# Optimization experiments

Measured on AMD Instinct MI355X. Metric: run time of the kernel, lower is better.

The kernel has to match this reference:

```python
import jax, jax.numpy as jnp
import numpy as np

N_EMBD = 1024
N_HEAD = 16
HEAD_DIM = N_EMBD // N_HEAD
EPS = 1e-5


def setup_inputs() -> dict:
    key = jax.random.key(0)
    ks = jax.random.split(key, 6)
    B, S, D = 2, 2048, N_EMBD
    s = 0.02
    return {
        "x": jax.random.normal(ks[0], (B, S, D), jnp.float32),
        "ln1_g": jnp.ones((D,), jnp.float32),
        "ln1_b": jnp.zeros((D,), jnp.float32),
        "w_attn": jax.random.normal(ks[1], (D, 3 * D), jnp.float32) * s,
        "b_attn": jnp.zeros((3 * D,), jnp.float32),
        "w_attn_proj": jax.random.normal(ks[2], (D, D), jnp.float32) * s,
        "b_attn_proj": jnp.zeros((D,), jnp.float32),
        "ln2_g": jnp.ones((D,), jnp.float32),
        "ln2_b": jnp.zeros((D,), jnp.float32),
        "w_fc": jax.random.normal(ks[3], (D, 4 * D), jnp.float32) * s,
        "b_fc": jnp.zeros((4 * D,), jnp.float32),
        "w_fc_proj": jax.random.normal(ks[4], (4 * D, D), jnp.float32) * s,
        "b_fc_proj": jnp.zeros((D,), jnp.float32),
    }


def _layernorm(x, g, b):
    mu = jnp.mean(x, axis=-1, keepdims=True)
    var = jnp.mean(jnp.square(x - mu), axis=-1, keepdims=True)
    return (x - mu) * jax.lax.rsqrt(var + EPS) * g + b


def _block(x, ln1_g, ln1_b, w_attn, b_attn, w_attn_proj, b_attn_proj,
           ln2_g, ln2_b, w_fc, b_fc, w_fc_proj, b_fc_proj):
    B, S, D = x.shape
    h = _layernorm(x, ln1_g, ln1_b)
    qkv = h @ w_attn + b_attn                       # [B,S,3D]
    q, k, v = jnp.split(qkv, 3, axis=-1)
    # [B,H,S,hd]
    q = q.reshape(B, S, N_HEAD, HEAD_DIM).transpose(0, 2, 1, 3)
    k = k.reshape(B, S, N_HEAD, HEAD_DIM).transpose(0, 2, 1, 3)
    v = v.reshape(B, S, N_HEAD, HEAD_DIM).transpose(0, 2, 1, 3)
    scores = jnp.einsum("bhqd,bhkd->bhqk", q, k) / jnp.sqrt(
        jnp.asarray(HEAD_DIM, x.dtype))
    causal = jnp.tril(jnp.ones((S, S), bool))
    scores = jnp.where(causal, scores, -jnp.inf)
    attn = jax.nn.softmax(scores, axis=-1)
    out = jnp.einsum("bhqk,bhkd->bhqd", attn, v)    # [B,H,S,hd]
    out = out.transpose(0, 2, 1, 3).reshape(B, S, D)
    x = x + (out @ w_attn_proj + b_attn_proj)
    h2 = _layernorm(x, ln2_g, ln2_b)
    m = jax.nn.gelu(h2 @ w_fc + b_fc, approximate=False)
    x = x + (m @ w_fc_proj + b_fc_proj)
    return x


def reference(x, ln1_g, ln1_b, w_attn, b_attn, w_attn_proj, b_attn_proj,
              ln2_g, ln2_b, w_fc, b_fc, w_fc_proj, b_fc_proj):
    return _block(x, ln1_g, ln1_b, w_attn, b_attn, w_attn_proj, b_attn_proj,
                  ln2_g, ln2_b, w_fc, b_fc, w_fc_proj, b_fc_proj)
```

## Files before the change

kernel.cpp:

```cpp
#include <hip/hip_runtime.h>
#include <hip/hip_bf16.h>
#include <math.h>

typedef __bf16 bf16_t;
typedef bf16_t bf16x8 __attribute__((ext_vector_type(8)));
typedef float f32x4 __attribute__((ext_vector_type(4)));
typedef unsigned short u16;
typedef u16 ushort8 __attribute__((ext_vector_type(8)));

static __device__ __forceinline__ u16 f2bf(float f) {
    unsigned u = __builtin_bit_cast(unsigned, f);
    u += 0x7FFFu + ((u >> 16) & 1u);
    return (u16)(u >> 16);
}

__global__ __launch_bounds__(256) void ln_kernel(
    const float* __restrict__ x, const float* __restrict__ g,
    const float* __restrict__ be, u16* __restrict__ out)
{
    const int row = blockIdx.x;
    const int tid = threadIdx.x;
    const float4 v = ((const float4*)(x + (long)row * 1024))[tid];
    float s = v.x + v.y + v.z + v.w;
#pragma unroll
    for (int d = 32; d >= 1; d >>= 1) s += __shfl_xor(s, d);
    __shared__ float r1[4], r2[4];
    if ((tid & 63) == 0) r1[tid >> 6] = s;
    __syncthreads();
    const float mean = (r1[0] + r1[1] + r1[2] + r1[3]) * (1.0f / 1024.0f);
    const float dx = v.x - mean, dy = v.y - mean, dz = v.z - mean, dw = v.w - mean;
    float sq = dx * dx + dy * dy + dz * dz + dw * dw;
#pragma unroll
    for (int d = 32; d >= 1; d >>= 1) sq += __shfl_xor(sq, d);
    if ((tid & 63) == 0) r2[tid >> 6] = sq;
    __syncthreads();
    const float var = (r2[0] + r2[1] + r2[2] + r2[3]) * (1.0f / 1024.0f);
    const float rstd = rsqrtf(var + 1e-5f);
    const float4 gg = ((const float4*)g)[tid];
    const float4 bb = ((const float4*)be)[tid];
    ushort4 o;
    o.x = f2bf(dx * rstd * gg.x + bb.x);
    o.y = f2bf(dy * rstd * gg.y + bb.y);
    o.z = f2bf(dz * rstd * gg.z + bb.z);
    o.w = f2bf(dw * rstd * gg.w + bb.w);
    *(ushort4*)&out[(long)row * 1024 + tid * 4] = o;
}

__global__ __launch_bounds__(256) void tcvt_kernel(
    const float* __restrict__ in, u16* __restrict__ outT, int R, int C)
{
    __shared__ float tile[32][33];
    const int tx = threadIdx.x, ty = threadIdx.y;
    const int c0 = blockIdx.x * 32, r0 = blockIdx.y * 32;
#pragma unroll
    for (int i = 0; i < 4; ++i)
        tile[ty + i * 8][tx] = in[(long)(r0 + ty + i * 8) * C + c0 + tx];
    __syncthreads();
#pragma unroll
    for (int i = 0; i < 4; ++i)
        outT[(long)(c0 + ty + i * 8) * R + r0 + tx] = f2bf(tile[tx][ty + i * 8]);
}

template <int BM, int EPI, int DP>
static __device__ __forceinline__ void gemm_body(
    const u16* __restrict__ A, const u16* __restrict__ Bt,
    const float* __restrict__ bias, const float* __restrict__ resid,
    void* __restrict__ C, int M, int N, int K)
{
    constexpr int WN = (BM == 128) ? 2 : 4;
    constexpr int MR = 4;
    constexpr int NR = 128 / WN / 16;
    constexpr int AI = BM / 64;
    constexpr int LPW = AI + 2;
    __shared__ __align__(16) u16 As[DP][BM * 32];
    __shared__ __align__(16) u16 Bs[DP][128 * 32];
    const int tid = threadIdx.x;
    const int lane = tid & 63;
    const int w = tid >> 6;
    const int wm = w / WN, wn = w % WN;
    const int nwg = gridDim.x * gridDim.y;
    const int flat = blockIdx.x + gridDim.x * blockIdx.y;
    const int work = (flat & 7) * (nwg >> 3) + (flat >> 3);
    const int bm = work % gridDim.x, bn = work / gridDim.x;
    f32x4 acc[MR][NR] = {};

    const u16* Ablk = A + (long)bm * BM * K;
    const u16* Bblk = Bt + (long)bn * 128 * K;
    const int nt = K >> 5;

    auto stage = [&](int buf, int kb) {
#pragma unroll
        for (int i = 0; i < AI; ++i) {
            const int o = (w * AI + i) * 512 + lane * 8;
            const int row = o >> 5, kk = o & 31;
            __builtin_amdgcn_global_load_lds(
                (const __attribute__((address_space(1))) void*)(Ablk + (long)row * K + kb + kk),
                (__attribute__((address_space(3))) void*)(&As[buf][(w * AI + i) * 512]),
                16, 0, 0);
        }
#pragma unroll
        for (int i = 0; i < 2; ++i) {
            const int o = (w * 2 + i) * 512 + lane * 8;
            const int row = o >> 5, kk = o & 31;
            __builtin_amdgcn_global_load_lds(
                (const __attribute__((address_space(1))) void*)(Bblk + (long)row * K + kb + kk),
                (__attribute__((address_space(3))) void*)(&Bs[buf][(w * 2 + i) * 512]),
                16, 0, 0);
        }
    };

#pragma unroll
    for (int s = 0; s < DP - 1; ++s) stage(s, s << 5);

    for (int t = 0; t < nt; ++t) {
        const int cur = t % DP;
        if (t + DP - 2 < nt) {
            asm volatile("s_waitcnt vmcnt(%0)" :: "i"((DP - 2) * LPW) : "memory");
        } else if (t + 1 < nt) {
            asm volatile("s_waitcnt vmcnt(%0)" :: "i"(LPW) : "memory");
        } else {
            asm volatile("s_waitcnt vmcnt(0)" ::: "memory");
        }
        __builtin_amdgcn_s_barrier();
        asm volatile("" ::: "memory");

        if (t + DP - 1 < nt) stage((t + DP - 1) % DP, (t + DP - 1) << 5);

        bf16x8 af[MR], bfr[NR];
#pragma unroll
        for (int m = 0; m < MR; ++m)
            af[m] = *(const bf16x8*)&As[cur][(wm * MR * 16 + m * 16 + (lane & 15)) * 32 + (lane >> 4) * 8];
#pragma unroll
        for (int n = 0; n < NR; ++n)
            bfr[n] = *(const bf16x8*)&Bs[cur][(wn * NR * 16 + n * 16 + (lane & 15)) * 32 + (lane >> 4) * 8];
#pragma unroll
        for (int m = 0; m < MR; ++m)
#pragma unroll
            for (int n = 0; n < NR; ++n)
                acc[m][n] = __builtin_amdgcn_mfma_f32_16x16x32_bf16(af[m], bfr[n], acc[m][n], 0, 0, 0);
        asm volatile("" ::: "memory");
    }

    const int rowBase = bm * BM + wm * MR * 16;
    const int colBase = bn * 128 + wn * NR * 16;
#pragma unroll
    for (int n = 0; n < NR; ++n) {
        const int col = colBase + n * 16 + (lane & 15);
        const float bv = bias[col];
#pragma unroll
        for (int m = 0; m < MR; ++m) {
#pragma unroll
            for (int r = 0; r < 4; ++r) {
                const int row = rowBase + m * 16 + (lane >> 4) * 4 + r;
                float v = acc[m][n][r] + bv;
                if constexpr (EPI == 1) {
                    const float u = v + 0.044715f * v * v * v;
                    v = v / (1.0f + __expf(-1.5957691216057308f * u));
                }
                if constexpr (EPI == 3) {
                    if (col < 1024) v *= 0.125f;
                }
                if constexpr (EPI == 2) {
                    ((float*)C)[(long)row * N + col] = v + resid[(long)row * N + col];
                } else {
                    ((u16*)C)[(long)row * N + col] = f2bf(v);
                }
            }
        }
    }
}

__global__ __launch_bounds__(256) void gemm_qkv(
    const u16* A, const u16* Bt, const float* bias, const float* resid,
    void* C, int M, int N, int K) { gemm_body<128, 3, 3>(A, Bt, bias, resid, C, M, N, K); }
__global__ __launch_bounds__(256) void gemm_fc(
    const u16* A, const u16* Bt, const float* bias, const float* resid,
    void* C, int M, int N, int K) { gemm_body<128, 1, 3>(A, Bt, bias, resid, C, M, N, K); }
__global__ __launch_bounds__(256) void gemm_ap(
    const u16* A, const u16* Bt, const float* bias, const float* resid,
    void* C, int M, int N, int K) { gemm_body<64, 2, 4>(A, Bt, bias, resid, C, M, N, K); }
__global__ __launch_bounds__(256) void gemm_fp(
    const u16* A, const u16* Bt, const float* bias, const float* resid,
    void* C, int M, int N, int K) { gemm_body<64, 2, 4>(A, Bt, bias, resid, C, M, N, K); }

__global__ __launch_bounds__(256) void attn_kernel(
    const u16* __restrict__ qkv, u16* __restrict__ outb)
{
    const int S = 2048;
    const int flat = blockIdx.x + 16 * blockIdx.y;
    const int work = (flat & 7) * 64 + (flat >> 3);
    const int ipair = work & 15;
    const int bh = work >> 4;
    const int b = bh >> 4, h = bh & 15;
    const int tid = threadIdx.x, lane = tid & 63, w = tid >> 6;
    __shared__ __align__(16) u16 Ks[2][64 * 72];
    __shared__ __align__(16) u16 Vs[2][64 * 72];
    __shared__ __align__(16) u16 Ps[4][16 * 72];

    const long base = (long)b * S * 3072;
    const int rstage = tid >> 3;
    const int cg = (tid & 7) * 8;
    const int sw = cg;
    const u16* kbase = qkv + base + 1024 + h * 64 + cg;
    const u16* vbase = qkv + base + 2048 + h * 64 + cg;

    for (int half = 0; half < 2; ++half) {
        const int qt = half ? 31 - ipair : ipair;
        const int q0 = qt * 64;

        bf16x8 qf[2];
        {
            const int qrow = q0 + w * 16 + (lane & 15);
#pragma unroll
            for (int c = 0; c < 2; ++c)
                qf[c] = *(const bf16x8*)&qkv[base + (long)qrow * 3072 + h * 64 + c * 32 + (lane >> 4) * 8];
        }

        f32x4 Of[4] = {};
        float m = -1e30f, l = 0.0f;

        ushort8 kr[2], vr[2];
#pragma unroll
        for (int it = 0; it < 2; ++it) {
            const long ro = (long)(it * 32 + rstage) * 3072;
            kr[it] = *(const ushort8*)&kbase[ro];
            vr[it] = *(const ushort8*)&vbase[ro];
        }
        __syncthreads();
#pragma unroll
        for (int it = 0; it < 2; ++it) {
            const int r = it * 32 + rstage;
            *(ushort8*)&Ks[0][r * 72 + cg] = kr[it];
#pragma unroll
            for (int j = 0; j < 8; ++j)
                Vs[0][(cg + j) * 72 + (r ^ sw)] = vr[it][j];
        }

        for (int kt = 0; kt <= qt; ++kt) {
            const int cur = kt & 1;
            if (kt < qt) {
#pragma unroll
                for (int it = 0; it < 2; ++it) {
                    const long ro = (long)((kt + 1) * 64 + it * 32 + rstage) * 3072;
                    kr[it] = *(const ushort8*)&kbase[ro];
                    vr[it] = *(const ushort8*)&vbase[ro];
                }
            }
            __syncthreads();

            f32x4 Sf[4] = {};
#pragma unroll
            for (int f = 0; f < 4; ++f) {
#pragma unroll
                for (int c = 0; c < 2; ++c) {
                    const bf16x8 kf = *(const bf16x8*)&Ks[cur][(f * 16 + (lane & 15)) * 72 + c * 32 + (lane >> 4) * 8];
                    Sf[f] = __builtin_amdgcn_mfma_f32_16x16x32_bf16(kf, qf[c], Sf[f], 0, 0, 0);
                }
            }
            if (kt == qt) {
                const int ql = w * 16 + (lane & 15);
#pragma unroll
                for (int f = 0; f < 4; ++f) {
#pragma unroll
                    for (int r = 0; r < 4; ++r) {
                        const int kvl = f * 16 + ((lane >> 4) << 2) + r;
                        if (kvl > ql) Sf[f][r] = -1e30f;
                    }
                }
            }
            float pmax = Sf[0][0];
#pragma unroll
            for (int f = 0; f < 4; ++f)
#pragma unroll
                for (int r = 0; r < 4; ++r) pmax = fmaxf(pmax, Sf[f][r]);
            if (!__all(pmax <= m + 8.0f)) {
                float pm = pmax;
                pm = fmaxf(pm, __shfl_xor(pm, 16));
                pm = fmaxf(pm, __shfl_xor(pm, 32));
                const float mnew = fmaxf(m, pm);
                const float sc = __expf(m - mnew);
                m = mnew;
                l *= sc;
                float sco[4];
#pragma unroll
                for (int r = 0; r < 4; ++r)
                    sco[r] = __shfl(sc, ((lane >> 4) << 2) + r);
#pragma unroll
                for (int f = 0; f < 4; ++f)
#pragma unroll
                    for (int r = 0; r < 4; ++r) Of[f][r] *= sco[r];
            }
            float osum = 0.0f;
#pragma unroll
            for (int f = 0; f < 4; ++f)
#pragma unroll
                for (int r = 0; r < 4; ++r) {
                    const float e = __expf(Sf[f][r] - m);
                    Sf[f][r] = e;
                    osum += e;
                }
            l += osum;
#pragma unroll
            for (int f = 0; f < 4; ++f) {
                const unsigned lo = (unsigned)f2bf(Sf[f][0]) | ((unsigned)f2bf(Sf[f][1]) << 16);
                const unsigned hi = (unsigned)f2bf(Sf[f][2]) | ((unsigned)f2bf(Sf[f][3]) << 16);
                uint2 pk; pk.x = lo; pk.y = hi;
                *(uint2*)&Ps[w][(lane & 15) * 72 + f * 16 + ((lane >> 4) << 2)] = pk;
            }
#pragma unroll
            for (int f = 0; f < 4; ++f) {
                const int hd = f * 16 + (lane & 15);
#pragma unroll
                for (int c = 0; c < 2; ++c) {
                    const int k0 = c * 32 + (lane >> 4) * 8;
                    const bf16x8 pa = *(const bf16x8*)&Ps[w][(lane & 15) * 72 + k0];
                    const bf16x8 vb = *(const bf16x8*)&Vs[cur][hd * 72 + (k0 ^ (hd & 56))];
                    Of[f] = __builtin_amdgcn_mfma_f32_16x16x32_bf16(pa, vb, Of[f], 0, 0, 0);
                }
            }
            if (kt < qt) {
#pragma unroll
                for (int it = 0; it < 2; ++it) {
                    const int r = it * 32 + rstage;
                    *(ushort8*)&Ks[cur ^ 1][r * 72 + cg] = kr[it];
#pragma unroll
                    for (int j = 0; j < 8; ++j)
                        Vs[cur ^ 1][(cg + j) * 72 + (r ^ sw)] = vr[it][j];
                }
            }
        }

        float lt = l;
        lt += __shfl_xor(lt, 16);
        lt += __shfl_xor(lt, 32);
        const float linv = 1.0f / lt;
        float inv[4];
#pragma unroll
        for (int r = 0; r < 4; ++r)
            inv[r] = __shfl(linv, ((lane >> 4) << 2) + r);
#pragma unroll
        for (int f = 0; f < 4; ++f) {
            const int col = h * 64 + f * 16 + (lane & 15);
#pragma unroll
            for (int r = 0; r < 4; ++r) {
                const int qrow = q0 + w * 16 + (lane >> 4) * 4 + r;
                outb[((long)b * S + qrow) * 1024 + col] = f2bf(Of[f][r] * inv[r]);
            }
        }
    }
}

extern "C" void kernel_launch(void* const* d_in, const int* in_sizes, int n_in,
                              void* d_out, int out_size, void* d_ws, size_t ws_size,
                              hipStream_t stream) {
    const float* x      = (const float*)d_in[0];
    const float* ln1_g  = (const float*)d_in[1];
    const float* ln1_b  = (const float*)d_in[2];
    const float* w_attn = (const float*)d_in[3];
    const float* b_attn = (const float*)d_in[4];
    const float* w_ap   = (const float*)d_in[5];
    const float* b_ap   = (const float*)d_in[6];
    const float* ln2_g  = (const float*)d_in[7];
    const float* ln2_b  = (const float*)d_in[8];
    const float* w_fc   = (const float*)d_in[9];
    const float* b_fc   = (const float*)d_in[10];
    const float* w_fp   = (const float*)d_in[11];
    const float* b_fp   = (const float*)d_in[12];
    float* out = (float*)d_out;

    const int R = 4096;
    char* p = (char*)d_ws;
    u16*   wTa  = (u16*)(p);
    u16*   wTap = (u16*)(p + 6291456);
    u16*   wTfc = (u16*)(p + 8388608);
    u16*   wTfp = (u16*)(p + 16777216);
    u16*   hao  = (u16*)(p + 25165824);
    u16*   qkv  = (u16*)(p + 33554432);
    u16*   mb   = hao;
    u16*   h2   = wTa;
    float* x1   = out;

    const dim3 tb(32, 8);
    tcvt_kernel<<<dim3(3072 / 32, 1024 / 32), tb, 0, stream>>>(w_attn, wTa, 1024, 3072);
    tcvt_kernel<<<dim3(1024 / 32, 1024 / 32), tb, 0, stream>>>(w_ap, wTap, 1024, 1024);
    tcvt_kernel<<<dim3(4096 / 32, 1024 / 32), tb, 0, stream>>>(w_fc, wTfc, 1024, 4096);
    tcvt_kernel<<<dim3(1024 / 32, 4096 / 32), tb, 0, stream>>>(w_fp, wTfp, 4096, 1024);

    ln_kernel<<<R, 256, 0, stream>>>(x, ln1_g, ln1_b, hao);
    gemm_qkv<<<dim3(32, 24), 256, 0, stream>>>(hao, wTa, b_attn, nullptr, qkv, R, 3072, 1024);
    attn_kernel<<<dim3(16, 32), 256, 0, stream>>>(qkv, hao);
    gemm_ap<<<dim3(64, 8), 256, 0, stream>>>(hao, wTap, b_ap, x, x1, R, 1024, 1024);
    ln_kernel<<<R, 256, 0, stream>>>(x1, ln2_g, ln2_b, h2);
    gemm_fc<<<dim3(32, 32), 256, 0, stream>>>(h2, wTfc, b_fc, nullptr, mb, R, 4096, 1024);
    gemm_fp<<<dim3(64, 8), 256, 0, stream>>>(mb, wTfp, b_fp, x1, out, R, 1024, 4096);
}
```

Before: 271.0 us.

## Stream B operand directly to registers in 64-row GEMMs, drop tile swizzle

The 64-row output-projection GEMMs get a new body. Each wave now loads its own 32 columns of B straight from global memory into registers with inline assembly, double-buffered, while only A is staged through LDS with two buffers instead of four. The 128-row GEMM is specialised to fixed constants, and the grouped workgroup remapping used for L2 locality is removed from both paths in favour of plain blockIdx order. This aims to cut LDS traffic and barrier cost for the skinny GEMMs, but it risks exposed global-load latency and worse L2 reuse without the swizzle.

New measurement: 271.3 us. About the same (+0.1%).

```diff
diff --git a/kernel.cpp b/kernel.cpp
--- a/kernel.cpp
+++ b/kernel.cpp
@@ -61,47 +61,36 @@
         outT[(long)(c0 + ty + i * 8) * R + r0 + tx] = f2bf(tile[tx][ty + i * 8]);
 }
 
-template <int BM, int EPI, int DP>
-static __device__ __forceinline__ void gemm_body(
+template <int EPI, int DP>
+static __device__ __forceinline__ void gemm128_body(
     const u16* __restrict__ A, const u16* __restrict__ Bt,
     const float* __restrict__ bias, const float* __restrict__ resid,
     void* __restrict__ C, int M, int N, int K)
 {
-    constexpr int WN = (BM == 128) ? 2 : 4;
-    constexpr int MR = 4;
-    constexpr int NR = 128 / WN / 16;
-    constexpr int AI = BM / 64;
-    constexpr int LPW = AI + 2;
-    __shared__ __align__(16) u16 As[DP][BM * 32];
+    constexpr int MR = 4, NR = 4;
+    constexpr int LPW = 4;
+    __shared__ __align__(16) u16 As[DP][128 * 32];
     __shared__ __align__(16) u16 Bs[DP][128 * 32];
     const int tid = threadIdx.x;
     const int lane = tid & 63;
     const int w = tid >> 6;
-    const int wm = w / WN, wn = w % WN;
-    const int nwg = gridDim.x * gridDim.y;
-    const int flat = blockIdx.x + gridDim.x * blockIdx.y;
-    const int work = (flat & 7) * (nwg >> 3) + (flat >> 3);
-    const int bm = work % gridDim.x, bn = work / gridDim.x;
+    const int wm = w >> 1, wn = w & 1;
+    const int bm = blockIdx.x, bn = blockIdx.y;
     f32x4 acc[MR][NR] = {};
 
-    const u16* Ablk = A + (long)bm * BM * K;
+    const u16* Ablk = A + (long)bm * 128 * K;
     const u16* Bblk = Bt + (long)bn * 128 * K;
     const int nt = K >> 5;
 
     auto stage = [&](int buf, int kb) {
 #pragma unroll
-        for (int i = 0; i < AI; ++i) {
-            const int o = (w * AI + i) * 512 + lane * 8;
+        for (int i = 0; i < 2; ++i) {
+            const int o = (w * 2 + i) * 512 + lane * 8;
             const int row = o >> 5, kk = o & 31;
             __builtin_amdgcn_global_load_lds(
                 (const __attribute__((address_space(1))) void*)(Ablk + (long)row * K + kb + kk),
-                (__attribute__((address_space(3))) void*)(&As[buf][(w * AI + i) * 512]),
+                (__attribute__((address_space(3))) void*)(&As[buf][(w * 2 + i) * 512]),
                 16, 0, 0);
-        }
-#pragma unroll
-        for (int i = 0; i < 2; ++i) {
-            const int o = (w * 2 + i) * 512 + lane * 8;
-            const int row = o >> 5, kk = o & 31;
             __builtin_amdgcn_global_load_lds(
                 (const __attribute__((address_space(1))) void*)(Bblk + (long)row * K + kb + kk),
                 (__attribute__((address_space(3))) void*)(&Bs[buf][(w * 2 + i) * 512]),
@@ -129,10 +118,10 @@
         bf16x8 af[MR], bfr[NR];
 #pragma unroll
         for (int m = 0; m < MR; ++m)
-            af[m] = *(const bf16x8*)&As[cur][(wm * MR * 16 + m * 16 + (lane & 15)) * 32 + (lane >> 4) * 8];
+            af[m] = *(const bf16x8*)&As[cur][(wm * 64 + m * 16 + (lane & 15)) * 32 + (lane >> 4) * 8];
 #pragma unroll
         for (int n = 0; n < NR; ++n)
-            bfr[n] = *(const bf16x8*)&Bs[cur][(wn * NR * 16 + n * 16 + (lane & 15)) * 32 + (lane >> 4) * 8];
+            bfr[n] = *(const bf16x8*)&Bs[cur][(wn * 64 + n * 16 + (lane & 15)) * 32 + (lane >> 4) * 8];
 #pragma unroll
         for (int m = 0; m < MR; ++m)
 #pragma unroll
@@ -141,8 +130,8 @@
         asm volatile("" ::: "memory");
     }
 
-    const int rowBase = bm * BM + wm * MR * 16;
-    const int colBase = bn * 128 + wn * NR * 16;
+    const int rowBase = bm * 128 + wm * 64;
+    const int colBase = bn * 128 + wn * 64;
 #pragma unroll
     for (int n = 0; n < NR; ++n) {
         const int col = colBase + n * 16 + (lane & 15);
@@ -170,18 +159,114 @@
     }
 }
 
+template <int EPI>
+static __device__ __forceinline__ void gemm64_body(
+    const u16* __restrict__ A, const u16* __restrict__ Bt,
+    const float* __restrict__ bias, const float* __restrict__ resid,
+    void* __restrict__ C, int M, int N, int K)
+{
+    constexpr int MR = 4, NR = 2;
+    __shared__ __align__(16) u16 As[2][64 * 32];
+    const int tid = threadIdx.x;
+    const int lane = tid & 63;
+    const int w = tid >> 6;
+    const int bm = blockIdx.x, bn = blockIdx.y;
+    f32x4 acc[MR][NR] = {};
+
+    const u16* Ablk = A + (long)bm * 64 * K;
+    const u16* Bblk = Bt + (long)bn * 128 * K;
+    const int nt = K >> 5;
+
+    const u16* bp0 = Bblk + (long)(w * 32 + (lane & 15)) * K + (lane >> 4) * 8;
+    const u16* bp1 = bp0 + 16 * K;
+
+    auto stageA = [&](int buf, int kb) {
+        const int o = w * 512 + lane * 8;
+        __builtin_amdgcn_global_load_lds(
+            (const __attribute__((address_space(1))) void*)(Ablk + (long)(o >> 5) * K + kb + (o & 31)),
+            (__attribute__((address_space(3))) void*)(&As[buf][w * 512]),
+            16, 0, 0);
+    };
+
+    ushort8 bBa[2], bBb[2];
+    stageA(0, 0);
+    __builtin_amdgcn_sched_barrier(0);
+    asm volatile("global_load_dwordx4 %0, %1, off" : "=v"(bBa[0]) : "v"(bp0));
+    asm volatile("global_load_dwordx4 %0, %1, off" : "=v"(bBa[1]) : "v"(bp1));
+
+    auto iter = [&](int t, ushort8* curB, ushort8* nxtB) {
+        asm volatile("s_waitcnt vmcnt(2)" ::: "memory");
+        __builtin_amdgcn_s_barrier();
+        asm volatile("" ::: "memory");
+        const bool more = (t + 1 < nt);
+        if (more) {
+            stageA((t + 1) & 1, (t + 1) << 5);
+            __builtin_amdgcn_sched_barrier(0);
+            const u16* a0 = bp0 + ((t + 1) << 5);
+            const u16* a1 = bp1 + ((t + 1) << 5);
+            asm volatile("global_load_dwordx4 %0, %1, off" : "=v"(nxtB[0]) : "v"(a0));
+            asm volatile("global_load_dwordx4 %0, %1, off" : "=v"(nxtB[1]) : "v"(a1));
+        }
+        bf16x8 af[MR];
+#pragma unroll
+        for (int m = 0; m < MR; ++m)
+            af[m] = *(const bf16x8*)&As[t & 1][(m * 16 + (lane & 15)) * 32 + (lane >> 4) * 8];
+        if (more) asm volatile("s_waitcnt vmcnt(3)" ::: "memory");
+        else      asm volatile("s_waitcnt vmcnt(0)" ::: "memory");
+        __builtin_amdgcn_sched_barrier(0);
+        const bf16x8 b0 = __builtin_bit_cast(bf16x8, curB[0]);
+        const bf16x8 b1 = __builtin_bit_cast(bf16x8, curB[1]);
+#pragma unroll
+        for (int m = 0; m < MR; ++m) {
+            acc[m][0] = __builtin_amdgcn_mfma_f32_16x16x32_bf16(af[m], b0, acc[m][0], 0, 0, 0);
+            acc[m][1] = __builtin_amdgcn_mfma_f32_16x16x32_bf16(af[m], b1, acc[m][1], 0, 0, 0);
+        }
+        asm volatile("" ::: "memory");
+    };
+
+    for (int t = 0; t < nt; t += 2) {
+        iter(t, bBa, bBb);
+        iter(t + 1, bBb, bBa);
+    }
+
+    const int rowBase = bm * 64;
+    const int colBase = bn * 128 + w * 32;
+#pragma unroll
+    for (int n = 0; n < NR; ++n) {
+        const int col = colBase + n * 16 + (lane & 15);
+        const float bv = bias[col];
+#pragma unroll
+        for (int m = 0; m < MR; ++m) {
+#pragma unroll
+            for (int r = 0; r < 4; ++r) {
+                const int row = rowBase + m * 16 + (lane >> 4) * 4 + r;
+                float v = acc[m][n][r] + bv;
+                if constexpr (EPI == 1) {
+                    const float u = v + 0.044715f * v * v * v;
+                    v = v / (1.0f + __expf(-1.5957691216057308f * u));
+                }
+                if constexpr (EPI == 2) {
+                    ((float*)C)[(long)row * N + col] = v + resid[(long)row * N + col];
+                } else {
+                    ((u16*)C)[(long)row * N + col] = f2bf(v);
+                }
+            }
+        }
+    }
+}
+
 __global__ __launch_bounds__(256) void gemm_qkv(
     const u16* A, const u16* Bt, const float* bias, const float* resid,
-    void* C, int M, int N, int K) { gemm_body<128, 3, 3>(A, Bt, bias, resid, C, M, N, K); }
+    void* C, int M, int N, int K) { gemm128_body<3, 3>(A, Bt, bias, resid, C, M, N, K); }
 __global__ __launch_bounds__(256) void gemm_fc(
     const u16* A, const u16* Bt, const float* bias, const float* resid,
-    void* C, int M, int N, int K) { gemm_body<128, 1, 3>(A, Bt, bias, resid, C, M, N, K); }
+    void* C, int M, int N, int K) { gemm128_body<1, 3>(A, Bt, bias, resid, C, M, N, K); }
 __global__ __launch_bounds__(256) void gemm_ap(
     const u16* A, const u16* Bt, const float* bias, const float* resid,
-    void* C, int M, int N, int K) { gemm_body<64, 2, 4>(A, Bt, bias, resid, C, M, N, K); }
+    void* C, int M, int N, int K) { gemm64_body<2>(A, Bt, bias, resid, C, M, N, K); }
 __global__ __launch_bounds__(256) void gemm_fp(
     const u16* A, const u16* Bt, const float* bias, const float* resid,
-    void* C, int M, int N, int K) { gemm_body<64, 2, 4>(A, Bt, bias, resid, C, M, N, K); }
+    void* C, int M, int N, int K) { gemm64_body<2>(A, Bt, bias, resid, C, M, N, K); }
 
 __global__ __launch_bounds__(256) void attn_kernel(
     const u16* __restrict__ qkv, u16* __restrict__ outb)
```
